# Optimization experiments

Measured on AMD Instinct MI355X. Metric: run time of the kernel, lower is better.

## Reference

```python
import jax, jax.numpy as jnp
import numpy as np

V_SIZE = 128000  # vocab size (v_size init arg)


def setup_inputs() -> dict:
    key = jax.random.key(0)
    k1, k2 = jax.random.split(key)
    # per-position scores -> weighting_scheme (softmax over seq dim)
    w_es = jax.random.normal(k1, (256, 2048), dtype=jnp.float32)
    # instance['x']: token ids in [0, v_size)
    x = jax.random.randint(k2, (256, 2048), 0, V_SIZE, dtype=jnp.int64)
    return {"w_es": w_es, "x": x}


def reference(w_es, x):
    # weighting_scheme(indices, w_es, instance): softmax over sequence positions
    weights = jax.nn.softmax(w_es, axis=-1)          # [B, S]
    B, S = weights.shape
    rows = jnp.arange(B)[:, None]                    # [B, 1] broadcast against [B, S]
    # scatter: w_a[b, x[b, i]] = weights[b, i]  (vectorized index_put)
    w_a = jnp.zeros((B, V_SIZE), dtype=weights.dtype).at[rows, x].set(weights)
    return (w_a, weights)
```

## Files before the change

### kernel.cpp

```cpp
#include <hip/hip_runtime.h>

#define BATCH 256
#define SEQ   2048
#define VOCAB 128000
#define HALF  64000
#define HSLOT 4096

typedef float v4f __attribute__((ext_vector_type(4)));
typedef int   v4i __attribute__((ext_vector_type(4)));
typedef float v2f __attribute__((ext_vector_type(2)));
typedef int   v2i __attribute__((ext_vector_type(2)));

#define LBAR() do { asm volatile("s_waitcnt lgkmcnt(0)" ::: "memory"); \
                    __builtin_amdgcn_s_barrier(); } while (0)

__device__ __forceinline__ int hash_v(int v) {
    return (int)(((unsigned)v * 2654435761u) >> 20);
}

__global__ __launch_bounds__(1024, 4)
void softmax_scatter_hash(const float* __restrict__ w_es,
                          const int*   __restrict__ x,
                          float* __restrict__ w_a,
                          float* __restrict__ w_out)
{
    __shared__ int      key[HSLOT];
    __shared__ int      val[HSLOT];
    __shared__ unsigned bm[HALF / 32];
    __shared__ float    red[32];

    const int bid = blockIdx.x;
    const int r = bid & (BATCH - 1);
    const int h = bid >> 8;
    const int t = threadIdx.x;
    const int lane = t & 63;
    const int wid  = t >> 6;

    {
        const v4i m1 = (v4i)(-1);
        ((v4i*)key)[t] = m1;
        ((v4i*)val)[t] = m1;
        if (t < (HALF / 32 / 4)) ((v4i*)bm)[t] = (v4i)(0);
    }

    const v2f a  = ((const v2f*)(w_es + (size_t)r * SEQ))[t];
    const v2i xv = ((const v2i*)(x    + (size_t)r * SEQ))[t];

    float m = fmaxf(a.x, a.y);
    #pragma unroll
    for (int off = 32; off > 0; off >>= 1)
        m = fmaxf(m, __shfl_down(m, off, 64));
    if (lane == 0) red[wid] = m;
    __syncthreads();
    m = red[0];
    #pragma unroll
    for (int k = 1; k < 16; ++k) m = fmaxf(m, red[k]);

    const int i0 = 2 * t;
    const int i1 = 2 * t + 1;
    const int v0 = xv.x - h * HALF;
    const int v1 = xv.y - h * HALF;
    const bool in0 = (unsigned)v0 < (unsigned)HALF;
    const bool in1 = (unsigned)v1 < (unsigned)HALF;

    if (in0) {
        atomicOr(&bm[v0 >> 5], 1u << (v0 & 31));
        int s = hash_v(v0);
        while (true) {
            int k = atomicCAS(&key[s], -1, v0);
            if (k == -1 || k == v0) break;
            s = (s + 1) & (HSLOT - 1);
        }
        atomicMax(&val[s], i0);
    }
    if (in1) {
        atomicOr(&bm[v1 >> 5], 1u << (v1 & 31));
        int s = hash_v(v1);
        while (true) {
            int k = atomicCAS(&key[s], -1, v1);
            if (k == -1 || k == v1) break;
            s = (s + 1) & (HSLOT - 1);
        }
        atomicMax(&val[s], i1);
    }

    const float e0 = __expf(a.x - m);
    const float e1 = __expf(a.y - m);
    float s = e0 + e1;
    #pragma unroll
    for (int off = 32; off > 0; off >>= 1)
        s += __shfl_down(s, off, 64);
    if (lane == 0) red[16 + wid] = s;
    __syncthreads();
    s = red[16];
    #pragma unroll
    for (int k = 1; k < 16; ++k) s += red[16 + k];

    const float inv = 1.0f / s;
    const float w0 = e0 * inv;
    const float w1 = e1 * inv;

    if (h == 0) {
        v2f wv; wv.x = w0; wv.y = w1;
        ((v2f*)(w_out + (size_t)r * SEQ))[t] = wv;
    }

    if (in0) {
        int sl = hash_v(v0);
        while (key[sl] != v0) sl = (sl + 1) & (HSLOT - 1);
        if (val[sl] == i0) val[sl] = __float_as_int(w0);
    }
    if (in1) {
        int sl = hash_v(v1);
        while (key[sl] != v1) sl = (sl + 1) & (HSLOT - 1);
        if (val[sl] == i1) val[sl] = __float_as_int(w1);
    }
    LBAR();

    float* gp = w_a + (size_t)r * VOCAB + h * HALF;
    for (int g = t; g < (HALF >> 2); g += 1024) {
        const unsigned word = bm[g >> 3];
        const unsigned nib  = (word >> ((g & 7) << 2)) & 0xFu;
        v4f o = (v4f)(0.0f);
        if (nib) {
            #pragma unroll
            for (int k = 0; k < 4; ++k) {
                if (nib & (1u << k)) {
                    const int v = (g << 2) + k;
                    int sl = hash_v(v);
                    while (key[sl] != v) sl = (sl + 1) & (HSLOT - 1);
                    o[k] = __int_as_float(val[sl]);
                }
            }
        }
        ((v4f*)gp)[g] = o;
    }
}

extern "C" void kernel_launch(void* const* d_in, const int* in_sizes, int n_in,
                              void* d_out, int out_size, void* d_ws, size_t ws_size,
                              hipStream_t stream) {
    const float* w_es = (const float*)d_in[0];
    const int*   x    = (const int*)d_in[1];

    float* out  = (float*)d_out;
    float* w_a  = out;
    float* w    = out + (size_t)BATCH * VOCAB;

    softmax_scatter_hash<<<2 * BATCH, 1024, 0, stream>>>(w_es, x, w_a, w);
}
```

Before: 138.2 us.

## Zero-fill output rows directly and scatter winning weights to global memory

```diff
diff --git a/kernel.cpp b/kernel.cpp
--- a/kernel.cpp
+++ b/kernel.cpp
@@ -19,15 +19,14 @@
 }
 
 __global__ __launch_bounds__(1024, 4)
-void softmax_scatter_hash(const float* __restrict__ w_es,
-                          const int*   __restrict__ x,
-                          float* __restrict__ w_a,
-                          float* __restrict__ w_out)
+void softmax_zero_then_scatter(const float* __restrict__ w_es,
+                               const int*   __restrict__ x,
+                               float* __restrict__ w_a,
+                               float* __restrict__ w_out)
 {
-    __shared__ int      key[HSLOT];
-    __shared__ int      val[HSLOT];
-    __shared__ unsigned bm[HALF / 32];
-    __shared__ float    red[32];
+    __shared__ int   key[HSLOT];
+    __shared__ int   val[HSLOT];
+    __shared__ float red[32];
 
     const int bid = blockIdx.x;
     const int r = bid & (BATCH - 1);
@@ -36,53 +35,33 @@
     const int lane = t & 63;
     const int wid  = t >> 6;
 
-    {
-        const v4i m1 = (v4i)(-1);
-        ((v4i*)key)[t] = m1;
-        ((v4i*)val)[t] = m1;
-        if (t < (HALF / 32 / 4)) ((v4i*)bm)[t] = (v4i)(0);
-    }
-
     const v2f a  = ((const v2f*)(w_es + (size_t)r * SEQ))[t];
     const v2i xv = ((const v2i*)(x    + (size_t)r * SEQ))[t];
+
+    ((v4i*)key)[t] = (v4i)(-1);
+    ((v4i*)val)[t] = (v4i)(-1);
+
+    __syncthreads();
+
+    v4f* gp4 = (v4f*)(w_a + (size_t)r * VOCAB + h * HALF);
+    {
+        const v4f z = (v4f)(0.0f);
+        #pragma unroll
+        for (int j = 0; j < 15; ++j)
+            gp4[j * 1024 + t] = z;
+        if (t < 640)
+            gp4[15 * 1024 + t] = z;
+    }
 
     float m = fmaxf(a.x, a.y);
     #pragma unroll
     for (int off = 32; off > 0; off >>= 1)
         m = fmaxf(m, __shfl_down(m, off, 64));
     if (lane == 0) red[wid] = m;
-    __syncthreads();
+    LBAR();
     m = red[0];
     #pragma unroll
     for (int k = 1; k < 16; ++k) m = fmaxf(m, red[k]);
-
-    const int i0 = 2 * t;
-    const int i1 = 2 * t + 1;
-    const int v0 = xv.x - h * HALF;
-    const int v1 = xv.y - h * HALF;
-    const bool in0 = (unsigned)v0 < (unsigned)HALF;
-    const bool in1 = (unsigned)v1 < (unsigned)HALF;
-
-    if (in0) {
-        atomicOr(&bm[v0 >> 5], 1u << (v0 & 31));
-        int s = hash_v(v0);
-        while (true) {
-            int k = atomicCAS(&key[s], -1, v0);
-            if (k == -1 || k == v0) break;
-            s = (s + 1) & (HSLOT - 1);
-        }
-        atomicMax(&val[s], i0);
-    }
-    if (in1) {
-        atomicOr(&bm[v1 >> 5], 1u << (v1 & 31));
-        int s = hash_v(v1);
-        while (true) {
-            int k = atomicCAS(&key[s], -1, v1);
-            if (k == -1 || k == v1) break;
-            s = (s + 1) & (HSLOT - 1);
-        }
-        atomicMax(&val[s], i1);
-    }
 
     const float e0 = __expf(a.x - m);
     const float e1 = __expf(a.y - m);
@@ -91,7 +70,7 @@
     for (int off = 32; off > 0; off >>= 1)
         s += __shfl_down(s, off, 64);
     if (lane == 0) red[16 + wid] = s;
-    __syncthreads();
+    LBAR();
     s = red[16];
     #pragma unroll
     for (int k = 1; k < 16; ++k) s += red[16 + k];
@@ -105,35 +84,44 @@
         ((v2f*)(w_out + (size_t)r * SEQ))[t] = wv;
     }
 
+    const int i0 = 2 * t;
+    const int i1 = 2 * t + 1;
+    const int v0 = xv.x - h * HALF;
+    const int v1 = xv.y - h * HALF;
+    const bool in0 = (unsigned)v0 < (unsigned)HALF;
+    const bool in1 = (unsigned)v1 < (unsigned)HALF;
+
+    if (in0) {
+        int sl = hash_v(v0);
+        while (true) {
+            int k = atomicCAS(&key[sl], -1, v0);
+            if (k == -1 || k == v0) break;
+            sl = (sl + 1) & (HSLOT - 1);
+        }
+        atomicMax(&val[sl], i0);
+    }
+    if (in1) {
+        int sl = hash_v(v1);
+        while (true) {
+            int k = atomicCAS(&key[sl], -1, v1);
+            if (k == -1 || k == v1) break;
+            sl = (sl + 1) & (HSLOT - 1);
+        }
+        atomicMax(&val[sl], i1);
+    }
+
+    __syncthreads();
+
+    float* gp = w_a + (size_t)r * VOCAB + h * HALF;
     if (in0) {
         int sl = hash_v(v0);
         while (key[sl] != v0) sl = (sl + 1) & (HSLOT - 1);
-        if (val[sl] == i0) val[sl] = __float_as_int(w0);
+        if (val[sl] == i0) gp[v0] = w0;
     }
     if (in1) {
         int sl = hash_v(v1);
         while (key[sl] != v1) sl = (sl + 1) & (HSLOT - 1);
-        if (val[sl] == i1) val[sl] = __float_as_int(w1);
-    }
-    LBAR();
-
-    float* gp = w_a + (size_t)r * VOCAB + h * HALF;
-    for (int g = t; g < (HALF >> 2); g += 1024) {
-        const unsigned word = bm[g >> 3];
-        const unsigned nib  = (word >> ((g & 7) << 2)) & 0xFu;
-        v4f o = (v4f)(0.0f);
-        if (nib) {
-            #pragma unroll
-            for (int k = 0; k < 4; ++k) {
-                if (nib & (1u << k)) {
-                    const int v = (g << 2) + k;
-                    int sl = hash_v(v);
-                    while (key[sl] != v) sl = (sl + 1) & (HSLOT - 1);
-                    o[k] = __int_as_float(val[sl]);
-                }
-            }
-        }
-        ((v4f*)gp)[g] = o;
+        if (val[sl] == i1) gp[v1] = w1;
     }
 }
 
@@ -147,5 +135,5 @@
     float* w_a  = out;
     float* w    = out + (size_t)BATCH * VOCAB;
 
-    softmax_scatter_hash<<<2 * BATCH, 1024, 0, stream>>>(w_es, x, w_a, w);
+    softmax_zero_then_scatter<<<2 * BATCH, 1024, 0, stream>>>(w_es, x, w_a, w);
 }
```

Result: no change. 138.2 us (-0.0%).
